# Optimization experiments

Hardware: AMD Instinct MI355X
Metric: run time of the kernel (lower is better)

The kernel has to match this reference:

```python
import jax, jax.numpy as jnp
import numpy as np

SEQ, BATCH, IN, HID, MID = 512, 64, 64, 512, 256


def setup_inputs() -> dict:
    key = jax.random.key(0)
    ks = jax.random.split(key, 8)
    concat_size = IN + 2 * HID  # 1088
    z_size = IN + MID  # 320
    sc = lambda n: 1.0 / np.sqrt(n)
    return {
        "x": jax.random.normal(ks[0], (SEQ, BATCH, IN), dtype=jnp.float32),
        "old_m": jax.random.normal(ks[1], (BATCH, HID), dtype=jnp.float32),
        "old_s": jnp.ones((BATCH, HID), dtype=jnp.float32),
        "W_z": jax.random.normal(ks[2], (MID, concat_size), dtype=jnp.float32) * sc(concat_size),
        "b_z": jnp.zeros((MID,), dtype=jnp.float32),
        "W_s": jax.random.normal(ks[3], (HID, z_size), dtype=jnp.float32) * sc(z_size),
        "b_s": jnp.zeros((HID,), dtype=jnp.float32),
        "W_m": jax.random.normal(ks[4], (HID, z_size), dtype=jnp.float32) * sc(z_size),
        "b_m": jnp.zeros((HID,), dtype=jnp.float32),
    }


def reference(x, old_m, old_s, W_z, b_z, W_s, b_s, W_m, b_m):
    def step(carry, x_t):
        m, s = carry  # [B, H] each
        z_inpt = jnp.concatenate([x_t, m, 1.0 / s], axis=-1)  # [B, IN+2H]
        z = jnp.concatenate([x_t, jnp.tanh(z_inpt @ W_z.T + b_z)], axis=-1)  # [B, IN+MID]
        new_s = s + jax.nn.sigmoid(z @ W_s.T + b_s)
        m_gate = jax.lax.stop_gradient(s / new_s)
        new_m = m_gate * m + (1.0 - m_gate) * jnp.tanh(z @ W_m.T + b_m)
        return (new_m, new_s), (new_m, new_s)

    _, (out_m, out_s) = jax.lax.scan(step, (old_m, old_s), x)
    return out_m, out_s
```

## Files before the change

kernel.cpp:

```cpp
#include <hip/hip_runtime.h>
#include <math.h>
#include <stdint.h>

#define SEQ    512
#define BATCH  64
#define IN_    64
#define HID    512
#define MID    256
#define CONCAT 1088
#define ZS     320
#define NW     4
#define QZ     64
#define L2E    1.4426950408889634f

typedef _Float16 h2t __attribute__((ext_vector_type(2)));

__device__ __forceinline__ float fdot2u(uint32_t a, uint32_t b, float c) {
    return __builtin_amdgcn_fdot2(__builtin_bit_cast(h2t, a),
                                  __builtin_bit_cast(h2t, b), c, false);
}
__device__ __forceinline__ uint32_t packrtn(float a, float b) {
    h2t h = { (_Float16)a, (_Float16)b };
    return __builtin_bit_cast(uint32_t, h);
}
template <int CTRL>
__device__ __forceinline__ float dpp_add(float v) {
    int o = __builtin_amdgcn_update_dpp(0, __builtin_bit_cast(int, v), CTRL, 0xF, 0xF, true);
    return v + __builtin_bit_cast(float, o);
}
template <int CTRL>
__device__ __forceinline__ float dpp_get(float v) {
    int o = __builtin_amdgcn_update_dpp(0, __builtin_bit_cast(int, v), CTRL, 0xF, 0xF, true);
    return __builtin_bit_cast(float, o);
}
__device__ __forceinline__ float red16(float v) {
    v = dpp_add<0xB1>(v);
    v = dpp_add<0x4E>(v);
    v = dpp_add<0x124>(v);
    v = dpp_add<0x128>(v);
    return v;
}
__device__ __forceinline__ float sw_add16(float v) {
    int o = __builtin_amdgcn_ds_swizzle(__builtin_bit_cast(int, v), 0x401F);
    return v + __builtin_bit_cast(float, o);
}
__device__ __forceinline__ float fexp2(float x) {
    float r;
    asm("v_exp_f32 %0, %1" : "=v"(r) : "v"(x));
    return r;
}
__device__ __forceinline__ float frcp(float x) { return __builtin_amdgcn_rcpf(x); }
__device__ __forceinline__ float fsigmoid(float x) {
    return frcp(1.f + fexp2(-x * L2E));
}
__device__ __forceinline__ float ftanh(float x) {
    return 1.f - 2.f * frcp(fexp2(x * (2.f * L2E)) + 1.f);
}
__device__ __forceinline__ int zidx(int k) { return (k / 17) * 20 + (k % 17); }

__device__ uint64_t g_px[(size_t)BATCH * 2 * NW * HID];

__global__ __launch_bounds__(512, 1)
void metamu9_kernel(const float* __restrict__ x,
                    const float* __restrict__ old_m,
                    const float* __restrict__ old_s,
                    const float* __restrict__ W_z,
                    const float* __restrict__ b_z,
                    const float* __restrict__ W_s,
                    const float* __restrict__ b_s,
                    const float* __restrict__ W_m,
                    const float* __restrict__ b_m,
                    float* __restrict__ out)
{
    const int bid = blockIdx.x;
    const int b   = bid & 63;
    const int w   = bid >> 6;
    const int tid = threadIdx.x;
    const int h   = tid;

    __shared__ __align__(16) uint32_t zin2[2][32 * 20];
    __shared__ __align__(16) uint32_t zvec2[2][40];

    const int g2 = tid >> 5, c2 = tid & 31;
    const int l  = tid & 1;

    uint32_t wA[4][17];
    #pragma unroll
    for (int r = 0; r < 4; ++r) {
        const float* p = W_z + (size_t)(QZ * w + 4 * g2 + r) * CONCAT + 34 * c2;
        #pragma unroll
        for (int i = 0; i < 17; ++i) {
            float2 a = *reinterpret_cast<const float2*>(p + 2 * i);
            wA[r][i] = packrtn(a.x, a.y);
        }
    }
    uint32_t wS0[20], wM0[20], wS1[20], wM1[20];
    {
        const int h0 = tid & ~1, h1 = tid | 1;
        const float* ps0 = W_s + (size_t)h0 * ZS;
        const float* pm0 = W_m + (size_t)h0 * ZS;
        const float* ps1 = W_s + (size_t)h1 * ZS;
        const float* pm1 = W_m + (size_t)h1 * ZS;
        #pragma unroll
        for (int i = 0; i < 4; ++i) {
            const int o = 16 * w + 8 * l + 2 * i;
            float2 a0 = *reinterpret_cast<const float2*>(ps0 + o);
            float2 b0 = *reinterpret_cast<const float2*>(pm0 + o);
            float2 a1 = *reinterpret_cast<const float2*>(ps1 + o);
            float2 b1 = *reinterpret_cast<const float2*>(pm1 + o);
            wS0[i] = packrtn(a0.x, a0.y); wM0[i] = packrtn(b0.x, b0.y);
            wS1[i] = packrtn(a1.x, a1.y); wM1[i] = packrtn(b1.x, b1.y);
        }
        #pragma unroll
        for (int i = 0; i < 16; ++i) {
            const int o = 64 + 64 * w + 32 * l + 2 * i;
            float2 a0 = *reinterpret_cast<const float2*>(ps0 + o);
            float2 b0 = *reinterpret_cast<const float2*>(pm0 + o);
            float2 a1 = *reinterpret_cast<const float2*>(ps1 + o);
            float2 b1 = *reinterpret_cast<const float2*>(pm1 + o);
            wS0[4 + i] = packrtn(a0.x, a0.y); wM0[4 + i] = packrtn(b0.x, b0.y);
            wS1[4 + i] = packrtn(a1.x, a1.y); wM1[4 + i] = packrtn(b1.x, b1.y);
        }
    }
    float bz[4];
    #pragma unroll
    for (int r = 0; r < 4; ++r) bz[r] = b_z[QZ * w + 4 * g2 + r];
    const float bsv = b_s[h], bmv = b_m[h];

    float sreg = old_s[b * HID + h];
    float mreg = old_m[b * HID + h];

    float2 xv = {0.f, 0.f};
    if (tid < 32) xv = *reinterpret_cast<const float2*>(x + (size_t)b * IN_ + 2 * tid);

    if (tid < 256) {
        float2 mv = *reinterpret_cast<const float2*>(old_m + b * HID + 2 * tid);
        zin2[0][zidx(32 + tid)] = packrtn(mv.x, mv.y);
    } else {
        const int j = tid - 256;
        float2 sv = *reinterpret_cast<const float2*>(old_s + b * HID + 2 * j);
        zin2[0][zidx(288 + j)] = packrtn(frcp(sv.x), frcp(sv.y));
    }
    if (tid < 32) zin2[0][zidx(tid)] = packrtn(xv.x, xv.y);
    if (tid >= 8 * w && tid < 8 * w + 8) zvec2[0][tid - 8 * w] = packrtn(xv.x, xv.y);
    __syncthreads();

    float* __restrict__ out_m = out;
    float* __restrict__ out_s = out + (size_t)SEQ * BATCH * HID;

    for (int t = 0; t < SEQ; ++t) {
        const int par = t & 1;
        const int np  = par ^ 1;
        const uint64_t want = (uint64_t)(t + 1);

        {
            uint32_t zf[17];
            const uint32_t* zc = &zin2[par][c2 * 20];
            #pragma unroll
            for (int i = 0; i < 4; ++i) {
                uint4 v = *reinterpret_cast<const uint4*>(zc + 4 * i);
                zf[4 * i] = v.x; zf[4 * i + 1] = v.y; zf[4 * i + 2] = v.z; zf[4 * i + 3] = v.w;
            }
            zf[16] = zc[16];
            float a0 = 0.f, a1 = 0.f, a2 = 0.f, a3 = 0.f;
            #pragma unroll
            for (int i = 0; i < 17; ++i) {
                a0 = fdot2u(wA[0][i], zf[i], a0);
                a1 = fdot2u(wA[1][i], zf[i], a1);
                a2 = fdot2u(wA[2][i], zf[i], a2);
                a3 = fdot2u(wA[3][i], zf[i], a3);
            }
            a0 = sw_add16(red16(a0));
            a1 = sw_add16(red16(a1));
            a2 = sw_add16(red16(a2));
            a3 = sw_add16(red16(a3));
            if (c2 == 0) {
                zvec2[par][8 + 2 * g2]     = packrtn(ftanh(a0 + bz[0]), ftanh(a1 + bz[1]));
                zvec2[par][8 + 2 * g2 + 1] = packrtn(ftanh(a2 + bz[2]), ftanh(a3 + bz[3]));
            }
        }
        __syncthreads();

        float as, am;
        {
            uint32_t zg[20];
            {
                uint4 v = *reinterpret_cast<const uint4*>(&zvec2[par][4 * l]);
                zg[0] = v.x; zg[1] = v.y; zg[2] = v.z; zg[3] = v.w;
            }
            const uint32_t* zc2 = &zvec2[par][8 + 16 * l];
            #pragma unroll
            for (int i = 0; i < 4; ++i) {
                uint4 v = *reinterpret_cast<const uint4*>(zc2 + 4 * i);
                zg[4 + 4 * i] = v.x; zg[5 + 4 * i] = v.y; zg[6 + 4 * i] = v.z; zg[7 + 4 * i] = v.w;
            }
            float as0 = 0.f, am0 = 0.f, as1 = 0.f, am1 = 0.f;
            #pragma unroll
            for (int i = 0; i < 20; ++i) {
                as0 = fdot2u(wS0[i], zg[i], as0);
                am0 = fdot2u(wM0[i], zg[i], am0);
                as1 = fdot2u(wS1[i], zg[i], as1);
                am1 = fdot2u(wM1[i], zg[i], am1);
            }
            as0 = dpp_add<0xB1>(as0);
            am0 = dpp_add<0xB1>(am0);
            as1 = dpp_add<0xB1>(as1);
            am1 = dpp_add<0xB1>(am1);
            as = l ? as1 : as0;
            am = l ? am1 : am0;
        }
        __hip_atomic_store(&g_px[(((size_t)b * 2 + par) * NW + w) * HID + h],
                           (want << 32) | (uint64_t)packrtn(as, am),
                           __ATOMIC_RELAXED, __HIP_MEMORY_SCOPE_AGENT);
        asm volatile("s_waitcnt vmcnt(0)" ::: "memory");

        if (tid < 32 && t + 1 < SEQ)
            xv = *reinterpret_cast<const float2*>(
                x + ((size_t)(t + 1) * BATCH + b) * IN_ + 2 * tid);

        {
            const size_t base = ((size_t)b * 2 + par) * NW;
            const uint64_t* s0 = &g_px[(base + ((w + 1) & 3)) * HID + h];
            const uint64_t* s1 = &g_px[(base + ((w + 2) & 3)) * HID + h];
            const uint64_t* s2 = &g_px[(base + ((w + 3) & 3)) * HID + h];
            uint64_t p0 = __hip_atomic_load(s0, __ATOMIC_RELAXED, __HIP_MEMORY_SCOPE_AGENT);
            uint64_t p1 = __hip_atomic_load(s1, __ATOMIC_RELAXED, __HIP_MEMORY_SCOPE_AGENT);
            uint64_t p2 = __hip_atomic_load(s2, __ATOMIC_RELAXED, __HIP_MEMORY_SCOPE_AGENT);
            bool r0 = (p0 >> 32) == want;
            bool r1 = (p1 >> 32) == want;
            bool r2 = (p2 >> 32) == want;
            while (!(r0 && r1 && r2)) {
                __builtin_amdgcn_s_sleep(1);
                if (!r0) { p0 = __hip_atomic_load(s0, __ATOMIC_RELAXED, __HIP_MEMORY_SCOPE_AGENT); }
                if (!r1) { p1 = __hip_atomic_load(s1, __ATOMIC_RELAXED, __HIP_MEMORY_SCOPE_AGENT); }
                if (!r2) { p2 = __hip_atomic_load(s2, __ATOMIC_RELAXED, __HIP_MEMORY_SCOPE_AGENT); }
                r0 = (p0 >> 32) == want;
                r1 = (p1 >> 32) == want;
                r2 = (p2 >> 32) == want;
            }
            h2t h0 = __builtin_bit_cast(h2t, (uint32_t)p0);
            h2t h1 = __builtin_bit_cast(h2t, (uint32_t)p1);
            h2t h2 = __builtin_bit_cast(h2t, (uint32_t)p2);
            as += (float)h0.x + (float)h1.x + (float)h2.x;
            am += (float)h0.y + (float)h1.y + (float)h2.y;
        }

        const float sig  = fsigmoid(as + bsv);
        const float ns   = sreg + sig;
        const float inv  = frcp(ns);
        const float gate = sreg * inv;
        const float nm   = gate * mreg + (1.f - gate) * ftanh(am + bmv);
        sreg = ns; mreg = nm;

        if ((h >> 7) == w) {
            const size_t o = ((size_t)t * BATCH + b) * HID + h;
            out_m[o] = nm;
            out_s[o] = ns;
        }

        const float nm_n  = dpp_get<0xB1>(nm);
        const float inv_n = dpp_get<0xB1>(inv);
        if ((tid & 1) == 0) {
            zin2[np][zidx(32 + (tid >> 1))]  = packrtn(nm, nm_n);
            zin2[np][zidx(288 + (tid >> 1))] = packrtn(inv, inv_n);
        }
        if (t + 1 < SEQ) {
            if (tid < 32) zin2[np][zidx(tid)] = packrtn(xv.x, xv.y);
            if (tid >= 8 * w && tid < 8 * w + 8)
                zvec2[np][tid - 8 * w] = packrtn(xv.x, xv.y);
        }
        __syncthreads();
    }
}

extern "C" void kernel_launch(void* const* d_in, const int* in_sizes, int n_in,
                              void* d_out, int out_size, void* d_ws, size_t ws_size,
                              hipStream_t stream) {
    const float* x     = (const float*)d_in[0];
    const float* old_m = (const float*)d_in[1];
    const float* old_s = (const float*)d_in[2];
    const float* W_z   = (const float*)d_in[3];
    const float* b_z   = (const float*)d_in[4];
    const float* W_s   = (const float*)d_in[5];
    const float* b_s   = (const float*)d_in[6];
    const float* W_m   = (const float*)d_in[7];
    const float* b_m   = (const float*)d_in[8];

    metamu9_kernel<<<dim3(BATCH * NW), dim3(512), 0, stream>>>(
        x, old_m, old_s, W_z, b_z, W_s, b_s, W_m, b_m, (float*)d_out);
}
```

Baseline: 1.041 ms.

## Process four batch rows per block to cut grid size and share weight registers

```diff
diff --git a/kernel.cpp b/kernel.cpp
--- a/kernel.cpp
+++ b/kernel.cpp
@@ -10,6 +10,8 @@
 #define CONCAT 1088
 #define ZS     320
 #define NW     4
+#define NB     4
+#define NG     16
 #define QZ     64
 #define L2E    1.4426950408889634f
 
@@ -50,36 +52,32 @@
     return r;
 }
 __device__ __forceinline__ float frcp(float x) { return __builtin_amdgcn_rcpf(x); }
-__device__ __forceinline__ float fsigmoid(float x) {
-    return frcp(1.f + fexp2(-x * L2E));
-}
-__device__ __forceinline__ float ftanh(float x) {
-    return 1.f - 2.f * frcp(fexp2(x * (2.f * L2E)) + 1.f);
-}
+__device__ __forceinline__ float fsigmoid(float x) { return frcp(1.f + fexp2(-x * L2E)); }
+__device__ __forceinline__ float ftanh(float x) { return 1.f - 2.f * frcp(fexp2(x * (2.f * L2E)) + 1.f); }
 __device__ __forceinline__ int zidx(int k) { return (k / 17) * 20 + (k % 17); }
 
 __device__ uint64_t g_px[(size_t)BATCH * 2 * NW * HID];
 
 __global__ __launch_bounds__(512, 1)
-void metamu9_kernel(const float* __restrict__ x,
-                    const float* __restrict__ old_m,
-                    const float* __restrict__ old_s,
-                    const float* __restrict__ W_z,
-                    const float* __restrict__ b_z,
-                    const float* __restrict__ W_s,
-                    const float* __restrict__ b_s,
-                    const float* __restrict__ W_m,
-                    const float* __restrict__ b_m,
-                    float* __restrict__ out)
+void metamu10_kernel(const float* __restrict__ x,
+                     const float* __restrict__ old_m,
+                     const float* __restrict__ old_s,
+                     const float* __restrict__ W_z,
+                     const float* __restrict__ b_z,
+                     const float* __restrict__ W_s,
+                     const float* __restrict__ b_s,
+                     const float* __restrict__ W_m,
+                     const float* __restrict__ b_m,
+                     float* __restrict__ out)
 {
     const int bid = blockIdx.x;
-    const int b   = bid & 63;
-    const int w   = bid >> 6;
+    const int gp  = bid & 15;
+    const int w   = bid >> 4;
     const int tid = threadIdx.x;
     const int h   = tid;
 
-    __shared__ __align__(16) uint32_t zin2[2][32 * 20];
-    __shared__ __align__(16) uint32_t zvec2[2][40];
+    __shared__ __align__(16) uint32_t zin2[2][NB][32 * 20];
+    __shared__ __align__(16) uint32_t zvec2[2][NB][40];
 
     const int g2 = tid >> 5, c2 = tid & 31;
     const int l  = tid & 1;
@@ -127,22 +125,34 @@
     for (int r = 0; r < 4; ++r) bz[r] = b_z[QZ * w + 4 * g2 + r];
     const float bsv = b_s[h], bmv = b_m[h];
 
-    float sreg = old_s[b * HID + h];
-    float mreg = old_m[b * HID + h];
-
+    float sreg[NB], mreg[NB];
+    #pragma unroll
+    for (int j = 0; j < NB; ++j) {
+        sreg[j] = old_s[(4 * gp + j) * HID + h];
+        mreg[j] = old_m[(4 * gp + j) * HID + h];
+    }
+
+    const int xj = tid >> 5, xe = tid & 31;
     float2 xv = {0.f, 0.f};
-    if (tid < 32) xv = *reinterpret_cast<const float2*>(x + (size_t)b * IN_ + 2 * tid);
-
-    if (tid < 256) {
-        float2 mv = *reinterpret_cast<const float2*>(old_m + b * HID + 2 * tid);
-        zin2[0][zidx(32 + tid)] = packrtn(mv.x, mv.y);
-    } else {
-        const int j = tid - 256;
-        float2 sv = *reinterpret_cast<const float2*>(old_s + b * HID + 2 * j);
-        zin2[0][zidx(288 + j)] = packrtn(frcp(sv.x), frcp(sv.y));
-    }
-    if (tid < 32) zin2[0][zidx(tid)] = packrtn(xv.x, xv.y);
-    if (tid >= 8 * w && tid < 8 * w + 8) zvec2[0][tid - 8 * w] = packrtn(xv.x, xv.y);
+    if (tid < 128)
+        xv = *reinterpret_cast<const float2*>(x + (size_t)(4 * gp + xj) * IN_ + 2 * xe);
+
+    #pragma unroll
+    for (int j = 0; j < NB; ++j) {
+        if (tid < 256) {
+            float2 mv = *reinterpret_cast<const float2*>(old_m + (4 * gp + j) * HID + 2 * tid);
+            zin2[0][j][zidx(32 + tid)] = packrtn(mv.x, mv.y);
+        } else {
+            const int jj = tid - 256;
+            float2 sv = *reinterpret_cast<const float2*>(old_s + (4 * gp + j) * HID + 2 * jj);
+            zin2[0][j][zidx(288 + jj)] = packrtn(frcp(sv.x), frcp(sv.y));
+        }
+    }
+    if (tid < 128) {
+        zin2[0][xj][zidx(xe)] = packrtn(xv.x, xv.y);
+        if (xe >= 8 * w && xe < 8 * w + 8)
+            zvec2[0][xj][xe - 8 * w] = packrtn(xv.x, xv.y);
+    }
     __syncthreads();
 
     float* __restrict__ out_m = out;
@@ -153,9 +163,10 @@
         const int np  = par ^ 1;
         const uint64_t want = (uint64_t)(t + 1);
 
-        {
+        #pragma unroll
+        for (int j = 0; j < NB; ++j) {
             uint32_t zf[17];
-            const uint32_t* zc = &zin2[par][c2 * 20];
+            const uint32_t* zc = &zin2[par][j][c2 * 20];
             #pragma unroll
             for (int i = 0; i < 4; ++i) {
                 uint4 v = *reinterpret_cast<const uint4*>(zc + 4 * i);
@@ -175,20 +186,21 @@
             a2 = sw_add16(red16(a2));
             a3 = sw_add16(red16(a3));
             if (c2 == 0) {
-                zvec2[par][8 + 2 * g2]     = packrtn(ftanh(a0 + bz[0]), ftanh(a1 + bz[1]));
-                zvec2[par][8 + 2 * g2 + 1] = packrtn(ftanh(a2 + bz[2]), ftanh(a3 + bz[3]));
+                zvec2[par][j][8 + 2 * g2]     = packrtn(ftanh(a0 + bz[0]), ftanh(a1 + bz[1]));
+                zvec2[par][j][8 + 2 * g2 + 1] = packrtn(ftanh(a2 + bz[2]), ftanh(a3 + bz[3]));
             }
         }
         __syncthreads();
 
-        float as, am;
-        {
+        float as[NB], am[NB];
+        #pragma unroll
+        for (int j = 0; j < NB; ++j) {
             uint32_t zg[20];
             {
-                uint4 v = *reinterpret_cast<const uint4*>(&zvec2[par][4 * l]);
+                uint4 v = *reinterpret_cast<const uint4*>(&zvec2[par][j][4 * l]);
                 zg[0] = v.x; zg[1] = v.y; zg[2] = v.z; zg[3] = v.w;
             }
-            const uint32_t* zc2 = &zvec2[par][8 + 16 * l];
+            const uint32_t* zc2 = &zvec2[par][j][8 + 16 * l];
             #pragma unroll
             for (int i = 0; i < 4; ++i) {
                 uint4 v = *reinterpret_cast<const uint4*>(zc2 + 4 * i);
@@ -206,68 +218,88 @@
             am0 = dpp_add<0xB1>(am0);
             as1 = dpp_add<0xB1>(as1);
             am1 = dpp_add<0xB1>(am1);
-            as = l ? as1 : as0;
-            am = l ? am1 : am0;
-        }
-        __hip_atomic_store(&g_px[(((size_t)b * 2 + par) * NW + w) * HID + h],
-                           (want << 32) | (uint64_t)packrtn(as, am),
-                           __ATOMIC_RELAXED, __HIP_MEMORY_SCOPE_AGENT);
+            as[j] = l ? as1 : as0;
+            am[j] = l ? am1 : am0;
+            __hip_atomic_store(
+                &g_px[(((size_t)(4 * gp + j) * 2 + par) * NW + w) * HID + h],
+                (want << 32) | (uint64_t)packrtn(as[j], am[j]),
+                __ATOMIC_RELAXED, __HIP_MEMORY_SCOPE_AGENT);
+        }
         asm volatile("s_waitcnt vmcnt(0)" ::: "memory");
 
-        if (tid < 32 && t + 1 < SEQ)
+        if (tid < 128 && t + 1 < SEQ)
             xv = *reinterpret_cast<const float2*>(
-                x + ((size_t)(t + 1) * BATCH + b) * IN_ + 2 * tid);
+                x + ((size_t)(t + 1) * BATCH + 4 * gp + xj) * IN_ + 2 * xe);
 
         {
-            const size_t base = ((size_t)b * 2 + par) * NW;
-            const uint64_t* s0 = &g_px[(base + ((w + 1) & 3)) * HID + h];
-            const uint64_t* s1 = &g_px[(base + ((w + 2) & 3)) * HID + h];
-            const uint64_t* s2 = &g_px[(base + ((w + 3) & 3)) * HID + h];
-            uint64_t p0 = __hip_atomic_load(s0, __ATOMIC_RELAXED, __HIP_MEMORY_SCOPE_AGENT);
-            uint64_t p1 = __hip_atomic_load(s1, __ATOMIC_RELAXED, __HIP_MEMORY_SCOPE_AGENT);
-            uint64_t p2 = __hip_atomic_load(s2, __ATOMIC_RELAXED, __HIP_MEMORY_SCOPE_AGENT);
-            bool r0 = (p0 >> 32) == want;
-            bool r1 = (p1 >> 32) == want;
-            bool r2 = (p2 >> 32) == want;
-            while (!(r0 && r1 && r2)) {
-                __builtin_amdgcn_s_sleep(1);
-                if (!r0) { p0 = __hip_atomic_load(s0, __ATOMIC_RELAXED, __HIP_MEMORY_SCOPE_AGENT); }
-                if (!r1) { p1 = __hip_atomic_load(s1, __ATOMIC_RELAXED, __HIP_MEMORY_SCOPE_AGENT); }
-                if (!r2) { p2 = __hip_atomic_load(s2, __ATOMIC_RELAXED, __HIP_MEMORY_SCOPE_AGENT); }
-                r0 = (p0 >> 32) == want;
-                r1 = (p1 >> 32) == want;
-                r2 = (p2 >> 32) == want;
-            }
-            h2t h0 = __builtin_bit_cast(h2t, (uint32_t)p0);
-            h2t h1 = __builtin_bit_cast(h2t, (uint32_t)p1);
-            h2t h2 = __builtin_bit_cast(h2t, (uint32_t)p2);
-            as += (float)h0.x + (float)h1.x + (float)h2.x;
-            am += (float)h0.y + (float)h1.y + (float)h2.y;
-        }
-
-        const float sig  = fsigmoid(as + bsv);
-        const float ns   = sreg + sig;
-        const float inv  = frcp(ns);
-        const float gate = sreg * inv;
-        const float nm   = gate * mreg + (1.f - gate) * ftanh(am + bmv);
-        sreg = ns; mreg = nm;
-
-        if ((h >> 7) == w) {
-            const size_t o = ((size_t)t * BATCH + b) * HID + h;
-            out_m[o] = nm;
-            out_s[o] = ns;
-        }
-
-        const float nm_n  = dpp_get<0xB1>(nm);
-        const float inv_n = dpp_get<0xB1>(inv);
-        if ((tid & 1) == 0) {
-            zin2[np][zidx(32 + (tid >> 1))]  = packrtn(nm, nm_n);
-            zin2[np][zidx(288 + (tid >> 1))] = packrtn(inv, inv_n);
-        }
-        if (t + 1 < SEQ) {
-            if (tid < 32) zin2[np][zidx(tid)] = packrtn(xv.x, xv.y);
-            if (tid >= 8 * w && tid < 8 * w + 8)
-                zvec2[np][tid - 8 * w] = packrtn(xv.x, xv.y);
+            const uint64_t* sp[NB][3];
+            uint64_t pw[NB][3];
+            bool rd[NB][3];
+            #pragma unroll
+            for (int j = 0; j < NB; ++j) {
+                const size_t basej = ((size_t)(4 * gp + j) * 2 + par) * NW;
+                #pragma unroll
+                for (int p = 0; p < 3; ++p) {
+                    sp[j][p] = &g_px[(basej + ((w + 1 + p) & 3)) * HID + h];
+                    pw[j][p] = __hip_atomic_load(sp[j][p], __ATOMIC_RELAXED, __HIP_MEMORY_SCOPE_AGENT);
+                    rd[j][p] = (pw[j][p] >> 32) == want;
+                }
+            }
+            bool all;
+            do {
+                all = true;
+                #pragma unroll
+                for (int j = 0; j < NB; ++j)
+                    #pragma unroll
+                    for (int p = 0; p < 3; ++p) all = all && rd[j][p];
+                if (!all) {
+                    __builtin_amdgcn_s_sleep(1);
+                    #pragma unroll
+                    for (int j = 0; j < NB; ++j)
+                        #pragma unroll
+                        for (int p = 0; p < 3; ++p)
+                            if (!rd[j][p]) {
+                                pw[j][p] = __hip_atomic_load(sp[j][p], __ATOMIC_RELAXED, __HIP_MEMORY_SCOPE_AGENT);
+                                rd[j][p] = (pw[j][p] >> 32) == want;
+                            }
+                }
+            } while (!all);
+            #pragma unroll
+            for (int j = 0; j < NB; ++j)
+                #pragma unroll
+                for (int p = 0; p < 3; ++p) {
+                    h2t hv = __builtin_bit_cast(h2t, (uint32_t)pw[j][p]);
+                    as[j] += (float)hv.x;
+                    am[j] += (float)hv.y;
+                }
+        }
+
+        #pragma unroll
+        for (int j = 0; j < NB; ++j) {
+            const float sig  = fsigmoid(as[j] + bsv);
+            const float ns   = sreg[j] + sig;
+            const float inv  = frcp(ns);
+            const float gate = sreg[j] * inv;
+            const float nm   = gate * mreg[j] + (1.f - gate) * ftanh(am[j] + bmv);
+            sreg[j] = ns; mreg[j] = nm;
+
+            if ((h >> 7) == w) {
+                const size_t o = ((size_t)t * BATCH + 4 * gp + j) * HID + h;
+                out_m[o] = nm;
+                out_s[o] = ns;
+            }
+
+            const float nm_n  = dpp_get<0xB1>(nm);
+            const float inv_n = dpp_get<0xB1>(inv);
+            if ((tid & 1) == 0) {
+                zin2[np][j][zidx(32 + (tid >> 1))]  = packrtn(nm, nm_n);
+                zin2[np][j][zidx(288 + (tid >> 1))] = packrtn(inv, inv_n);
+            }
+        }
+        if (t + 1 < SEQ && tid < 128) {
+            zin2[np][xj][zidx(xe)] = packrtn(xv.x, xv.y);
+            if (xe >= 8 * w && xe < 8 * w + 8)
+                zvec2[np][xj][xe - 8 * w] = packrtn(xv.x, xv.y);
         }
         __syncthreads();
     }
@@ -286,6 +318,6 @@
     const float* W_m   = (const float*)d_in[7];
     const float* b_m   = (const float*)d_in[8];
 
-    metamu9_kernel<<<dim3(BATCH * NW), dim3(512), 0, stream>>>(
+    metamu10_kernel<<<dim3(NG * NW), dim3(512), 0, stream>>>(
         x, old_m, old_s, W_z, b_z, W_s, b_s, W_m, b_m, (float*)d_out);
 }
```

Result: slower. 2.771 ms (+166.1%).

## Process two batch rows per block to overlap cross-block exchange latency

Applied to the files above, without the earlier changes.

```diff
diff --git a/kernel.cpp b/kernel.cpp
--- a/kernel.cpp
+++ b/kernel.cpp
@@ -50,36 +50,140 @@
     return r;
 }
 __device__ __forceinline__ float frcp(float x) { return __builtin_amdgcn_rcpf(x); }
-__device__ __forceinline__ float fsigmoid(float x) {
-    return frcp(1.f + fexp2(-x * L2E));
-}
-__device__ __forceinline__ float ftanh(float x) {
-    return 1.f - 2.f * frcp(fexp2(x * (2.f * L2E)) + 1.f);
-}
+__device__ __forceinline__ float fsigmoid(float x) { return frcp(1.f + fexp2(-x * L2E)); }
+__device__ __forceinline__ float ftanh(float x) { return 1.f - 2.f * frcp(fexp2(x * (2.f * L2E)) + 1.f); }
 __device__ __forceinline__ int zidx(int k) { return (k / 17) * 20 + (k % 17); }
 
 __device__ uint64_t g_px[(size_t)BATCH * 2 * NW * HID];
 
+#define PHASE_A(PAR, J)                                                         \
+    do {                                                                        \
+        uint32_t zf_[17];                                                       \
+        const uint32_t* zc_ = &zin2[PAR][J][c2 * 20];                           \
+        _Pragma("unroll")                                                       \
+        for (int i_ = 0; i_ < 4; ++i_) {                                        \
+            uint4 v_ = *reinterpret_cast<const uint4*>(zc_ + 4 * i_);           \
+            zf_[4*i_] = v_.x; zf_[4*i_+1] = v_.y;                               \
+            zf_[4*i_+2] = v_.z; zf_[4*i_+3] = v_.w;                             \
+        }                                                                       \
+        zf_[16] = zc_[16];                                                      \
+        float a0_ = 0.f, a1_ = 0.f, a2_ = 0.f, a3_ = 0.f;                       \
+        _Pragma("unroll")                                                       \
+        for (int i_ = 0; i_ < 17; ++i_) {                                       \
+            a0_ = fdot2u(wA[0][i_], zf_[i_], a0_);                              \
+            a1_ = fdot2u(wA[1][i_], zf_[i_], a1_);                              \
+            a2_ = fdot2u(wA[2][i_], zf_[i_], a2_);                              \
+            a3_ = fdot2u(wA[3][i_], zf_[i_], a3_);                              \
+        }                                                                       \
+        a0_ = sw_add16(red16(a0_));                                             \
+        a1_ = sw_add16(red16(a1_));                                             \
+        a2_ = sw_add16(red16(a2_));                                             \
+        a3_ = sw_add16(red16(a3_));                                             \
+        if (c2 == 0) {                                                          \
+            zvec2[PAR][J][8 + 2*g2]     = packrtn(ftanh(a0_ + bz[0]), ftanh(a1_ + bz[1])); \
+            zvec2[PAR][J][8 + 2*g2 + 1] = packrtn(ftanh(a2_ + bz[2]), ftanh(a3_ + bz[3])); \
+        }                                                                       \
+    } while (0)
+
+#define PHASE_B(PAR, J, AS, AM)                                                 \
+    do {                                                                        \
+        uint32_t zg_[20];                                                       \
+        {                                                                       \
+            uint4 v_ = *reinterpret_cast<const uint4*>(&zvec2[PAR][J][4 * l]);  \
+            zg_[0] = v_.x; zg_[1] = v_.y; zg_[2] = v_.z; zg_[3] = v_.w;         \
+        }                                                                       \
+        const uint32_t* zc2_ = &zvec2[PAR][J][8 + 16 * l];                      \
+        _Pragma("unroll")                                                       \
+        for (int i_ = 0; i_ < 4; ++i_) {                                        \
+            uint4 v_ = *reinterpret_cast<const uint4*>(zc2_ + 4 * i_);          \
+            zg_[4+4*i_] = v_.x; zg_[5+4*i_] = v_.y;                             \
+            zg_[6+4*i_] = v_.z; zg_[7+4*i_] = v_.w;                             \
+        }                                                                       \
+        float xs0_ = 0.f, xm0_ = 0.f, xs1_ = 0.f, xm1_ = 0.f;                   \
+        _Pragma("unroll")                                                       \
+        for (int i_ = 0; i_ < 20; ++i_) {                                       \
+            xs0_ = fdot2u(wS0[i_], zg_[i_], xs0_);                              \
+            xm0_ = fdot2u(wM0[i_], zg_[i_], xm0_);                              \
+            xs1_ = fdot2u(wS1[i_], zg_[i_], xs1_);                              \
+            xm1_ = fdot2u(wM1[i_], zg_[i_], xm1_);                              \
+        }                                                                       \
+        xs0_ = dpp_add<0xB1>(xs0_);                                             \
+        xm0_ = dpp_add<0xB1>(xm0_);                                             \
+        xs1_ = dpp_add<0xB1>(xs1_);                                             \
+        xm1_ = dpp_add<0xB1>(xm1_);                                             \
+        AS = l ? xs1_ : xs0_;                                                   \
+        AM = l ? xm1_ : xm0_;                                                   \
+        __hip_atomic_store(                                                     \
+            &g_px[(((size_t)(2*gp + J) * 2 + par) * NW + w) * HID + h],         \
+            (want << 32) | (uint64_t)packrtn(AS, AM),                           \
+            __ATOMIC_RELAXED, __HIP_MEMORY_SCOPE_AGENT);                        \
+    } while (0)
+
+#define POLL_FIN(PAR, NP, J, AS, AM)                                            \
+    do {                                                                        \
+        const size_t base_ = ((size_t)(2*gp + J) * 2 + PAR) * NW;               \
+        const uint64_t* s0_ = &g_px[(base_ + ((w + 1) & 3)) * HID + h];         \
+        const uint64_t* s1_ = &g_px[(base_ + ((w + 2) & 3)) * HID + h];         \
+        const uint64_t* s2_ = &g_px[(base_ + ((w + 3) & 3)) * HID + h];         \
+        uint64_t p0_ = __hip_atomic_load(s0_, __ATOMIC_RELAXED, __HIP_MEMORY_SCOPE_AGENT); \
+        uint64_t p1_ = __hip_atomic_load(s1_, __ATOMIC_RELAXED, __HIP_MEMORY_SCOPE_AGENT); \
+        uint64_t p2_ = __hip_atomic_load(s2_, __ATOMIC_RELAXED, __HIP_MEMORY_SCOPE_AGENT); \
+        bool r0_ = (p0_ >> 32) == want;                                         \
+        bool r1_ = (p1_ >> 32) == want;                                         \
+        bool r2_ = (p2_ >> 32) == want;                                         \
+        while (!(r0_ && r1_ && r2_)) {                                          \
+            __builtin_amdgcn_s_sleep(1);                                        \
+            if (!r0_) { p0_ = __hip_atomic_load(s0_, __ATOMIC_RELAXED, __HIP_MEMORY_SCOPE_AGENT); } \
+            if (!r1_) { p1_ = __hip_atomic_load(s1_, __ATOMIC_RELAXED, __HIP_MEMORY_SCOPE_AGENT); } \
+            if (!r2_) { p2_ = __hip_atomic_load(s2_, __ATOMIC_RELAXED, __HIP_MEMORY_SCOPE_AGENT); } \
+            r0_ = (p0_ >> 32) == want;                                          \
+            r1_ = (p1_ >> 32) == want;                                          \
+            r2_ = (p2_ >> 32) == want;                                          \
+        }                                                                       \
+        h2t h0_ = __builtin_bit_cast(h2t, (uint32_t)p0_);                       \
+        h2t h1_ = __builtin_bit_cast(h2t, (uint32_t)p1_);                       \
+        h2t h2_ = __builtin_bit_cast(h2t, (uint32_t)p2_);                       \
+        AS += (float)h0_.x + (float)h1_.x + (float)h2_.x;                       \
+        AM += (float)h0_.y + (float)h1_.y + (float)h2_.y;                       \
+        const float sig_  = fsigmoid(AS + bsv);                                 \
+        const float ns_   = sreg##J + sig_;                                     \
+        const float inv_  = frcp(ns_);                                          \
+        const float gate_ = sreg##J * inv_;                                     \
+        const float nm_   = gate_ * mreg##J + (1.f - gate_) * ftanh(AM + bmv);  \
+        sreg##J = ns_; mreg##J = nm_;                                           \
+        if ((h >> 7) == w) {                                                    \
+            const size_t o_ = ((size_t)t * BATCH + 2*gp + J) * HID + h;         \
+            out_m[o_] = nm_;                                                    \
+            out_s[o_] = ns_;                                                    \
+        }                                                                       \
+        const float nmn_  = dpp_get<0xB1>(nm_);                                 \
+        const float invn_ = dpp_get<0xB1>(inv_);                                \
+        if ((tid & 1) == 0) {                                                   \
+            zin2[NP][J][zidx(32 + (tid >> 1))]  = packrtn(nm_, nmn_);           \
+            zin2[NP][J][zidx(288 + (tid >> 1))] = packrtn(inv_, invn_);         \
+        }                                                                       \
+    } while (0)
+
 __global__ __launch_bounds__(512, 1)
-void metamu9_kernel(const float* __restrict__ x,
-                    const float* __restrict__ old_m,
-                    const float* __restrict__ old_s,
-                    const float* __restrict__ W_z,
-                    const float* __restrict__ b_z,
-                    const float* __restrict__ W_s,
-                    const float* __restrict__ b_s,
-                    const float* __restrict__ W_m,
-                    const float* __restrict__ b_m,
-                    float* __restrict__ out)
+void metamu12_kernel(const float* __restrict__ x,
+                     const float* __restrict__ old_m,
+                     const float* __restrict__ old_s,
+                     const float* __restrict__ W_z,
+                     const float* __restrict__ b_z,
+                     const float* __restrict__ W_s,
+                     const float* __restrict__ b_s,
+                     const float* __restrict__ W_m,
+                     const float* __restrict__ b_m,
+                     float* __restrict__ out)
 {
     const int bid = blockIdx.x;
-    const int b   = bid & 63;
-    const int w   = bid >> 6;
+    const int gp  = bid & 31;
+    const int w   = bid >> 5;
     const int tid = threadIdx.x;
     const int h   = tid;
 
-    __shared__ __align__(16) uint32_t zin2[2][32 * 20];
-    __shared__ __align__(16) uint32_t zvec2[2][40];
+    __shared__ __align__(16) uint32_t zin2[2][2][32 * 20];
+    __shared__ __align__(16) uint32_t zvec2[2][2][40];
 
     const int g2 = tid >> 5, c2 = tid & 31;
     const int l  = tid & 1;
@@ -127,22 +231,32 @@
     for (int r = 0; r < 4; ++r) bz[r] = b_z[QZ * w + 4 * g2 + r];
     const float bsv = b_s[h], bmv = b_m[h];
 
-    float sreg = old_s[b * HID + h];
-    float mreg = old_m[b * HID + h];
-
+    float sreg0 = old_s[(2 * gp + 0) * HID + h];
+    float mreg0 = old_m[(2 * gp + 0) * HID + h];
+    float sreg1 = old_s[(2 * gp + 1) * HID + h];
+    float mreg1 = old_m[(2 * gp + 1) * HID + h];
+
+    const int xj = tid >> 5, xe = tid & 31;
     float2 xv = {0.f, 0.f};
-    if (tid < 32) xv = *reinterpret_cast<const float2*>(x + (size_t)b * IN_ + 2 * tid);
-
-    if (tid < 256) {
-        float2 mv = *reinterpret_cast<const float2*>(old_m + b * HID + 2 * tid);
-        zin2[0][zidx(32 + tid)] = packrtn(mv.x, mv.y);
-    } else {
-        const int j = tid - 256;
-        float2 sv = *reinterpret_cast<const float2*>(old_s + b * HID + 2 * j);
-        zin2[0][zidx(288 + j)] = packrtn(frcp(sv.x), frcp(sv.y));
-    }
-    if (tid < 32) zin2[0][zidx(tid)] = packrtn(xv.x, xv.y);
-    if (tid >= 8 * w && tid < 8 * w + 8) zvec2[0][tid - 8 * w] = packrtn(xv.x, xv.y);
+    if (tid < 64)
+        xv = *reinterpret_cast<const float2*>(x + (size_t)(2 * gp + xj) * IN_ + 2 * xe);
+
+    #pragma unroll
+    for (int j = 0; j < 2; ++j) {
+        if (tid < 256) {
+            float2 mv = *reinterpret_cast<const float2*>(old_m + (2 * gp + j) * HID + 2 * tid);
+            zin2[0][j][zidx(32 + tid)] = packrtn(mv.x, mv.y);
+        } else {
+            const int jj = tid - 256;
+            float2 sv = *reinterpret_cast<const float2*>(old_s + (2 * gp + j) * HID + 2 * jj);
+            zin2[0][j][zidx(288 + jj)] = packrtn(frcp(sv.x), frcp(sv.y));
+        }
+    }
+    if (tid < 64) {
+        zin2[0][xj][zidx(xe)] = packrtn(xv.x, xv.y);
+        if (xe >= 8 * w && xe < 8 * w + 8)
+            zvec2[0][xj][xe - 8 * w] = packrtn(xv.x, xv.y);
+    }
     __syncthreads();
 
     float* __restrict__ out_m = out;
@@ -153,121 +267,31 @@
         const int np  = par ^ 1;
         const uint64_t want = (uint64_t)(t + 1);
 
-        {
-            uint32_t zf[17];
-            const uint32_t* zc = &zin2[par][c2 * 20];
-            #pragma unroll
-            for (int i = 0; i < 4; ++i) {
-                uint4 v = *reinterpret_cast<const uint4*>(zc + 4 * i);
-                zf[4 * i] = v.x; zf[4 * i + 1] = v.y; zf[4 * i + 2] = v.z; zf[4 * i + 3] = v.w;
-            }
-            zf[16] = zc[16];
-            float a0 = 0.f, a1 = 0.f, a2 = 0.f, a3 = 0.f;
-            #pragma unroll
-            for (int i = 0; i < 17; ++i) {
-                a0 = fdot2u(wA[0][i], zf[i], a0);
-                a1 = fdot2u(wA[1][i], zf[i], a1);
-                a2 = fdot2u(wA[2][i], zf[i], a2);
-                a3 = fdot2u(wA[3][i], zf[i], a3);
-            }
-            a0 = sw_add16(red16(a0));
-            a1 = sw_add16(red16(a1));
-            a2 = sw_add16(red16(a2));
-            a3 = sw_add16(red16(a3));
-            if (c2 == 0) {
-                zvec2[par][8 + 2 * g2]     = packrtn(ftanh(a0 + bz[0]), ftanh(a1 + bz[1]));
-                zvec2[par][8 + 2 * g2 + 1] = packrtn(ftanh(a2 + bz[2]), ftanh(a3 + bz[3]));
-            }
-        }
+        PHASE_A(par, 0);
         __syncthreads();
 
-        float as, am;
-        {
-            uint32_t zg[20];
-            {
-                uint4 v = *reinterpret_cast<const uint4*>(&zvec2[par][4 * l]);
-                zg[0] = v.x; zg[1] = v.y; zg[2] = v.z; zg[3] = v.w;
-            }
-            const uint32_t* zc2 = &zvec2[par][8 + 16 * l];
-            #pragma unroll
-            for (int i = 0; i < 4; ++i) {
-                uint4 v = *reinterpret_cast<const uint4*>(zc2 + 4 * i);
-                zg[4 + 4 * i] = v.x; zg[5 + 4 * i] = v.y; zg[6 + 4 * i] = v.z; zg[7 + 4 * i] = v.w;
-            }
-            float as0 = 0.f, am0 = 0.f, as1 = 0.f, am1 = 0.f;
-            #pragma unroll
-            for (int i = 0; i < 20; ++i) {
-                as0 = fdot2u(wS0[i], zg[i], as0);
-                am0 = fdot2u(wM0[i], zg[i], am0);
-                as1 = fdot2u(wS1[i], zg[i], as1);
-                am1 = fdot2u(wM1[i], zg[i], am1);
-            }
-            as0 = dpp_add<0xB1>(as0);
-            am0 = dpp_add<0xB1>(am0);
-            as1 = dpp_add<0xB1>(as1);
-            am1 = dpp_add<0xB1>(am1);
-            as = l ? as1 : as0;
-            am = l ? am1 : am0;
-        }
-        __hip_atomic_store(&g_px[(((size_t)b * 2 + par) * NW + w) * HID + h],
-                           (want << 32) | (uint64_t)packrtn(as, am),
-                           __ATOMIC_RELAXED, __HIP_MEMORY_SCOPE_AGENT);
+        float as0, am0;
+        PHASE_B(par, 0, as0, am0);
+
+        PHASE_A(par, 1);
+        __syncthreads();
+
+        float as1, am1;
+        PHASE_B(par, 1, as1, am1);
+
         asm volatile("s_waitcnt vmcnt(0)" ::: "memory");
 
-        if (tid < 32 && t + 1 < SEQ)
+        if (tid < 64 && t + 1 < SEQ)
             xv = *reinterpret_cast<const float2*>(
-                x + ((size_t)(t + 1) * BATCH + b) * IN_ + 2 * tid);
-
-        {
-            const size_t base = ((size_t)b * 2 + par) * NW;
-            const uint64_t* s0 = &g_px[(base + ((w + 1) & 3)) * HID + h];
-            const uint64_t* s1 = &g_px[(base + ((w + 2) & 3)) * HID + h];
-            const uint64_t* s2 = &g_px[(base + ((w + 3) & 3)) * HID + h];
-            uint64_t p0 = __hip_atomic_load(s0, __ATOMIC_RELAXED, __HIP_MEMORY_SCOPE_AGENT);
-            uint64_t p1 = __hip_atomic_load(s1, __ATOMIC_RELAXED, __HIP_MEMORY_SCOPE_AGENT);
-            uint64_t p2 = __hip_atomic_load(s2, __ATOMIC_RELAXED, __HIP_MEMORY_SCOPE_AGENT);
-            bool r0 = (p0 >> 32) == want;
-            bool r1 = (p1 >> 32) == want;
-            bool r2 = (p2 >> 32) == want;
-            while (!(r0 && r1 && r2)) {
-                __builtin_amdgcn_s_sleep(1);
-                if (!r0) { p0 = __hip_atomic_load(s0, __ATOMIC_RELAXED, __HIP_MEMORY_SCOPE_AGENT); }
-                if (!r1) { p1 = __hip_atomic_load(s1, __ATOMIC_RELAXED, __HIP_MEMORY_SCOPE_AGENT); }
-                if (!r2) { p2 = __hip_atomic_load(s2, __ATOMIC_RELAXED, __HIP_MEMORY_SCOPE_AGENT); }
-                r0 = (p0 >> 32) == want;
-                r1 = (p1 >> 32) == want;
-                r2 = (p2 >> 32) == want;
-            }
-            h2t h0 = __builtin_bit_cast(h2t, (uint32_t)p0);
-            h2t h1 = __builtin_bit_cast(h2t, (uint32_t)p1);
-            h2t h2 = __builtin_bit_cast(h2t, (uint32_t)p2);
-            as += (float)h0.x + (float)h1.x + (float)h2.x;
-            am += (float)h0.y + (float)h1.y + (float)h2.y;
-        }
-
-        const float sig  = fsigmoid(as + bsv);
-        const float ns   = sreg + sig;
-        const float inv  = frcp(ns);
-        const float gate = sreg * inv;
-        const float nm   = gate * mreg + (1.f - gate) * ftanh(am + bmv);
-        sreg = ns; mreg = nm;
-
-        if ((h >> 7) == w) {
-            const size_t o = ((size_t)t * BATCH + b) * HID + h;
-            out_m[o] = nm;
-            out_s[o] = ns;
-        }
-
-        const float nm_n  = dpp_get<0xB1>(nm);
-        const float inv_n = dpp_get<0xB1>(inv);
-        if ((tid & 1) == 0) {
-            zin2[np][zidx(32 + (tid >> 1))]  = packrtn(nm, nm_n);
-            zin2[np][zidx(288 + (tid >> 1))] = packrtn(inv, inv_n);
-        }
-        if (t + 1 < SEQ) {
-            if (tid < 32) zin2[np][zidx(tid)] = packrtn(xv.x, xv.y);
-            if (tid >= 8 * w && tid < 8 * w + 8)
-                zvec2[np][tid - 8 * w] = packrtn(xv.x, xv.y);
+                x + ((size_t)(t + 1) * BATCH + 2 * gp + xj) * IN_ + 2 * xe);
+
+        POLL_FIN(par, np, 0, as0, am0);
+        POLL_FIN(par, np, 1, as1, am1);
+
+        if (t + 1 < SEQ && tid < 64) {
+            zin2[np][xj][zidx(xe)] = packrtn(xv.x, xv.y);
+            if (xe >= 8 * w && xe < 8 * w + 8)
+                zvec2[np][xj][xe - 8 * w] = packrtn(xv.x, xv.y);
         }
         __syncthreads();
     }
@@ -286,6 +310,6 @@
     const float* W_m   = (const float*)d_in[7];
     const float* b_m   = (const float*)d_in[8];
 
-    metamu9_kernel<<<dim3(BATCH * NW), dim3(512), 0, stream>>>(
+    metamu12_kernel<<<dim3(32 * NW), dim3(512), 0, stream>>>(
         x, old_m, old_s, W_z, b_z, W_s, b_s, W_m, b_m, (float*)d_out);
 }
```

After: 1.682 ms. 61.5% more time.
